# Kernel tuning notes

Measured on AMD Instinct MI355X. Metric: run time of the kernel, lower is better.

The kernel has to match this reference:

```python
import jax, jax.numpy as jnp
import numpy as np

# dims: M=512 new tokens, N=2048 model dim, D=128 head dim, H=16 heads,
# L=4096 cache length, P=2048 cache write offset

def setup_inputs() -> dict:
    key = jax.random.key(0)
    k0, k1, k2, k3 = jax.random.split(key, 4)
    M, N, D, L = 512, 2048, 128, 4096
    X = jax.random.normal(k0, (M, N), jnp.float32)
    # scale weights ~1/sqrt(N) so projections have unit-ish scale
    W_qkv = jax.random.normal(k1, (N, 3 * N), jnp.float32) * (N ** -0.5)
    H = N // D
    cache_K = jax.random.normal(k2, (H, L, D), jnp.float32)
    # realistic cache state: keys stored in cache are RMS-normalized
    cache_K = cache_K * jax.lax.rsqrt(jnp.mean(cache_K * cache_K, axis=-1, keepdims=True))
    cache_V = jax.random.normal(k3, (H, L, D), jnp.float32)
    return {"X": X, "W_qkv": W_qkv, "cache_K": cache_K, "cache_V": cache_V, "P": 2048}


def reference(X, W_qkv, cache_K, cache_V, P):
    M = X.shape[0]
    H, L, D = cache_K.shape
    qkv = X @ W_qkv                              # [M, 3N]
    q, k, v = jnp.split(qkv, 3, axis=-1)         # each [M, N]
    q = q.reshape(M, H, D).transpose(1, 0, 2)    # [H, M, D]
    k = k.reshape(M, H, D).transpose(1, 0, 2)
    v = v.reshape(M, H, D).transpose(1, 0, 2)
    # RMS-style normalization (no learned gain, no eps in original)
    q = q * jax.lax.rsqrt(jnp.mean(q * q, axis=-1, keepdims=True))
    k = k * jax.lax.rsqrt(jnp.mean(k * k, axis=-1, keepdims=True))
    # scatter-update into KV cache at position P
    Kc = jax.lax.dynamic_update_slice(cache_K, k, (0, P, 0))  # [H, L, D]
    Vc = jax.lax.dynamic_update_slice(cache_V, v, (0, P, 0))
    # unmasked, unscaled attention over the full cache (faithful to original:
    # plain exp/sum, no max-subtraction, no 1/sqrt(D))
    scores = jnp.einsum('hmd,hld->hml', q, Kc)   # [H, M, L]
    w = jnp.exp(scores)
    w = w / jnp.sum(w, axis=-1, keepdims=True)
    out = jnp.einsum('hml,hld->hmd', w, Vc)      # [H, M, D]
    return out.transpose(1, 0, 2).reshape(M, H * D)
```

## Files before the change

### kernel.cpp

```cpp
#include <hip/hip_runtime.h>
#include <math.h>

typedef _Float16 half_t;
typedef _Float16 half8 __attribute__((ext_vector_type(8)));
typedef _Float16 half4_t __attribute__((ext_vector_type(4)));
typedef _Float16 half2_t __attribute__((ext_vector_type(2)));
typedef float floatx4 __attribute__((ext_vector_type(4)));

#define M_TOK 512
#define N_DIM 2048
#define D_HEAD 128
#define H_HEADS 16
#define L_CACHE 4096
#define THREE_N 6144
#define NCHUNK 16
#define LCHUNK 256

__global__ __launch_bounds__(256) void prep_kernel(const float* __restrict__ cV,
                                                   const float* __restrict__ W,
                                                   const float* __restrict__ X,
                                                   half_t* __restrict__ V16T,
                                                   half_t* __restrict__ W16T,
                                                   half_t* __restrict__ X16) {
    __shared__ half_t tile[128 * 36];
    int b = blockIdx.x;
    int t = threadIdx.x;

    if (b < 1024) {
        size_t i = ((size_t)b * 256 + t) * 4;
        float4 v = *(const float4*)(X + i);
        half4_t h = {(half_t)v.x, (half_t)v.y, (half_t)v.z, (half_t)v.w};
        *(half4_t*)(X16 + i) = h;
        return;
    }
    b -= 1024;
    if (b < 2048) {
        int h = b >> 7;
        int rem = b & 127;
        int l0 = (rem >> 2) * 128, d0 = (rem & 3) * 32;
        {
            int row = t >> 1, q = (t & 1) * 16;
            const float* src = cV + ((size_t)h * L_CACHE + l0 + row) * D_HEAD + d0 + q;
#pragma unroll
            for (int i = 0; i < 4; ++i) {
                float4 v = *(const float4*)(src + 4 * i);
                half4_t hv = {(half_t)v.x, (half_t)v.y, (half_t)v.z, (half_t)v.w};
                *(half4_t*)&tile[row * 36 + q + 4 * i] = hv;
            }
        }
        __syncthreads();
        {
            int drow = t >> 3, seg = (t & 7) * 16;
#pragma unroll
            for (int j = 0; j < 2; ++j) {
                half8 o;
#pragma unroll
                for (int kk = 0; kk < 8; ++kk)
                    o[kk] = tile[(seg + j * 8 + kk) * 36 + drow];
                *(half8*)(V16T + ((size_t)h * D_HEAD + d0 + drow) * L_CACHE + l0 + seg + j * 8) = o;
            }
        }
        return;
    }
    b -= 2048;
    {
        int kt = b / 192, nt = b % 192;
        int k0 = kt * 128, n0 = nt * 32;
        {
            int row = t >> 1, q = (t & 1) * 16;
            const float* src = W + (size_t)(k0 + row) * THREE_N + n0 + q;
#pragma unroll
            for (int i = 0; i < 4; ++i) {
                float4 v = *(const float4*)(src + 4 * i);
                half4_t hv = {(half_t)v.x, (half_t)v.y, (half_t)v.z, (half_t)v.w};
                *(half4_t*)&tile[row * 36 + q + 4 * i] = hv;
            }
        }
        __syncthreads();
        {
            int nrow = t >> 3, seg = (t & 7) * 16;
#pragma unroll
            for (int j = 0; j < 2; ++j) {
                half8 o;
#pragma unroll
                for (int kk = 0; kk < 8; ++kk)
                    o[kk] = tile[(seg + j * 8 + kk) * 36 + nrow];
                *(half8*)(W16T + (size_t)(n0 + nrow) * N_DIM + k0 + seg + j * 8) = o;
            }
        }
    }
}

__global__ __launch_bounds__(256) void gemm_fused_kernel(const half_t* __restrict__ X16,
                                                         const half_t* __restrict__ W16T,
                                                         const int* __restrict__ Pp,
                                                         half_t* __restrict__ Q16,
                                                         float* __restrict__ cacheK,
                                                         half_t* __restrict__ V16T) {
    __shared__ half_t smem[64 * 72 + 128 * 72];
    __shared__ float ssbuf[4][32];
    half_t* As = smem;
    half_t* Bs = smem + 64 * 72;
    half_t* Vt = smem;
    const int t = threadIdx.x;
    const int wid = t >> 6, lane = t & 63;
    const int quad = lane >> 4, ln = lane & 15;
    const int bx = blockIdx.x, by = blockIdx.y;
    const int m0 = by * 64, n0 = bx * 128;
    const int wm = (wid >> 1) * 32, wn = (wid & 1) * 64;

    floatx4 acc[2][4] = {};

    const int ar = t >> 3, ag = (t & 7) * 8;
    const int br = t >> 3, bg = (t & 7) * 8;

    for (int k0 = 0; k0 < N_DIM; k0 += 64) {
        __syncthreads();
#pragma unroll
        for (int p = 0; p < 2; ++p) {
            int r = ar + p * 32;
            *(half8*)&As[r * 72 + ag] =
                *(const half8*)(X16 + (size_t)(m0 + r) * N_DIM + k0 + ag);
        }
#pragma unroll
        for (int p = 0; p < 4; ++p) {
            int r = br + p * 32;
            *(half8*)&Bs[r * 72 + bg] =
                *(const half8*)(W16T + (size_t)(n0 + r) * N_DIM + k0 + bg);
        }
        __syncthreads();
#pragma unroll
        for (int kt = 0; kt < 2; ++kt) {
            half8 a[2], b[4];
#pragma unroll
            for (int i = 0; i < 2; ++i)
                a[i] = *(half8*)&As[(wm + i * 16 + ln) * 72 + kt * 32 + quad * 8];
#pragma unroll
            for (int j = 0; j < 4; ++j)
                b[j] = *(half8*)&Bs[(wn + j * 16 + ln) * 72 + kt * 32 + quad * 8];
#pragma unroll
            for (int i = 0; i < 2; ++i)
#pragma unroll
                for (int j = 0; j < 4; ++j)
                    acc[i][j] = __builtin_amdgcn_mfma_f32_16x16x32_f16(a[i], b[j], acc[i][j], 0, 0, 0);
        }
    }

    const int seg = bx >> 4, h = bx & 15;
    const int P = *Pp;

    if (seg < 2) {
        float ss[2][4], scale[2][4];
#pragma unroll
        for (int i = 0; i < 2; ++i)
#pragma unroll
            for (int r = 0; r < 4; ++r) {
                float s = 0.f;
#pragma unroll
                for (int j = 0; j < 4; ++j) s += acc[i][j][r] * acc[i][j][r];
#pragma unroll
                for (int msk = 1; msk < 16; msk <<= 1) s += __shfl_xor(s, msk, 64);
                ss[i][r] = s;
            }
        if (ln == 0) {
#pragma unroll
            for (int i = 0; i < 2; ++i)
#pragma unroll
                for (int r = 0; r < 4; ++r)
                    ssbuf[wid][i * 16 + quad * 4 + r] = ss[i][r];
        }
        __syncthreads();
#pragma unroll
        for (int i = 0; i < 2; ++i)
#pragma unroll
            for (int r = 0; r < 4; ++r)
                scale[i][r] =
                    rsqrtf((ss[i][r] + ssbuf[wid ^ 1][i * 16 + quad * 4 + r]) * (1.0f / 128.0f));
#pragma unroll
        for (int i = 0; i < 2; ++i) {
            int mbase = m0 + wm + i * 16 + quad * 4;
#pragma unroll
            for (int j = 0; j < 4; ++j) {
                int col = wn + j * 16 + ln;
#pragma unroll
                for (int r = 0; r < 4; ++r) {
                    int m = mbase + r;
                    float v = acc[i][j][r] * scale[i][r];
                    if (seg == 0)
                        Q16[((size_t)h * M_TOK + m) * D_HEAD + col] = (half_t)v;
                    else
                        cacheK[((size_t)h * L_CACHE + P + m) * D_HEAD + col] = v;
                }
            }
        }
    } else {
        __syncthreads();
#pragma unroll
        for (int i = 0; i < 2; ++i) {
            int mbase = wm + i * 16 + quad * 4;
#pragma unroll
            for (int j = 0; j < 4; ++j) {
                int d = wn + j * 16 + ln;
#pragma unroll
                for (int r = 0; r < 4; ++r)
                    Vt[d * 72 + mbase + r] = (half_t)acc[i][j][r];
            }
        }
        __syncthreads();
#pragma unroll
        for (int p = 0; p < 4; ++p) {
            int s = p * 256 + t;
            int d = s >> 3, sg = s & 7;
            *(half8*)(V16T + ((size_t)h * D_HEAD + d) * L_CACHE + P + m0 + sg * 8) =
                *(half8*)&Vt[d * 72 + sg * 8];
        }
    }
}

__global__ __launch_bounds__(256) void attn_partial_kernel(const half_t* __restrict__ Q16,
                                                           const float* __restrict__ cacheK,
                                                           const half_t* __restrict__ V16T,
                                                           half_t* __restrict__ Opart,
                                                           float* __restrict__ mstat,
                                                           float* __restrict__ lstat) {
    __shared__ half_t Ks[64 * 136];
    __shared__ half_t Vs[128 * 72];
    __shared__ half_t Ps[4 * 16 * 72];
    const int t = threadIdx.x, w = t >> 6, lane = t & 63;
    const int quad = lane >> 4, ln = lane & 15;
    const int f = blockIdx.x;
    const int pair = (f >> 5) * 8 + (f & 7);
    const int c = pair >> 4, h = pair & 15;
    const int mb = ((f >> 3) & 3) * 128;
    const half_t* Qh = Q16 + (size_t)h * M_TOK * D_HEAD;
    const float* Kh = cacheK + (size_t)h * L_CACHE * D_HEAD;
    const half_t* Vh = V16T + (size_t)h * D_HEAD * L_CACHE;

    half8 qf[2][4];
#pragma unroll
    for (int s = 0; s < 2; ++s) {
        int m0 = mb + s * 64 + w * 16;
#pragma unroll
        for (int dt = 0; dt < 4; ++dt)
            qf[s][dt] = *(const half8*)(Qh + (size_t)(m0 + ln) * D_HEAD + dt * 32 + quad * 8);
    }

    floatx4 oacc[2][8] = {};
    float mrow[2][4], lrow[2][4];
#pragma unroll
    for (int s = 0; s < 2; ++s)
#pragma unroll
        for (int r = 0; r < 4; ++r) { mrow[s][r] = -INFINITY; lrow[s][r] = 0.f; }

    half_t* Pw = Ps + w * (16 * 72);

    for (int l0 = c * LCHUNK; l0 < (c + 1) * LCHUNK; l0 += 64) {
        __syncthreads();
        {
            int lr = t >> 4, ch = (t & 15) * 8;
#pragma unroll
            for (int p = 0; p < 4; ++p, lr += 16) {
                const float* src = Kh + (size_t)(l0 + lr) * D_HEAD + ch;
                float4 a = *(const float4*)src;
                float4 bq = *(const float4*)(src + 4);
                half8 hv = {(half_t)a.x, (half_t)a.y, (half_t)a.z, (half_t)a.w,
                            (half_t)bq.x, (half_t)bq.y, (half_t)bq.z, (half_t)bq.w};
                *(half8*)&Ks[lr * 136 + ch] = hv;
            }
        }
        {
            int dr = t >> 3, ch = t & 7;
#pragma unroll
            for (int p = 0; p < 4; ++p, dr += 32)
                *(half8*)&Vs[dr * 72 + ch * 8] =
                    *(const half8*)(Vh + (size_t)dr * L_CACHE + l0 + ch * 8);
        }
        __syncthreads();

#pragma unroll
        for (int s = 0; s < 2; ++s) {
            floatx4 sacc[4] = {};
#pragma unroll
            for (int nt = 0; nt < 4; ++nt)
#pragma unroll
                for (int dt = 0; dt < 4; ++dt) {
                    half8 b = *(half8*)&Ks[(nt * 16 + ln) * 136 + dt * 32 + quad * 8];
                    sacc[nt] = __builtin_amdgcn_mfma_f32_16x16x32_f16(qf[s][dt], b, sacc[nt], 0, 0, 0);
                }

            float alpha[4];
#pragma unroll
            for (int r = 0; r < 4; ++r) {
                float mx = fmaxf(fmaxf(sacc[0][r], sacc[1][r]), fmaxf(sacc[2][r], sacc[3][r]));
#pragma unroll
                for (int msk = 8; msk; msk >>= 1) mx = fmaxf(mx, __shfl_xor(mx, msk, 16));
                float mnew = fmaxf(mrow[s][r], mx);
                alpha[r] = __expf(mrow[s][r] - mnew);
                mrow[s][r] = mnew;
                float psum = 0.f;
#pragma unroll
                for (int nt = 0; nt < 4; ++nt) {
                    float p = __expf(sacc[nt][r] - mnew);
                    sacc[nt][r] = p;
                    psum += p;
                }
#pragma unroll
                for (int msk = 8; msk; msk >>= 1) psum += __shfl_xor(psum, msk, 16);
                lrow[s][r] = lrow[s][r] * alpha[r] + psum;
            }

#pragma unroll
            for (int nt = 0; nt < 4; ++nt)
#pragma unroll
                for (int r = 0; r < 4; ++r)
                    Pw[(quad * 4 + r) * 72 + nt * 16 + ln] = (half_t)sacc[nt][r];

#pragma unroll
            for (int nt8 = 0; nt8 < 8; ++nt8)
#pragma unroll
                for (int r = 0; r < 4; ++r)
                    oacc[s][nt8][r] *= alpha[r];

#pragma unroll
            for (int kt = 0; kt < 2; ++kt) {
                half8 a = *(half8*)&Pw[ln * 72 + kt * 32 + quad * 8];
#pragma unroll
                for (int nt8 = 0; nt8 < 8; ++nt8) {
                    half8 b = *(half8*)&Vs[(nt8 * 16 + ln) * 72 + kt * 32 + quad * 8];
                    oacc[s][nt8] = __builtin_amdgcn_mfma_f32_16x16x32_f16(a, b, oacc[s][nt8], 0, 0, 0);
                }
            }
        }
    }

    half_t* Oc = Opart + ((size_t)(c * H_HEADS + h) * M_TOK) * D_HEAD;
    float* ms = mstat + (size_t)(c * H_HEADS + h) * M_TOK;
    float* ls = lstat + (size_t)(c * H_HEADS + h) * M_TOK;
#pragma unroll
    for (int s = 0; s < 2; ++s) {
        int m0 = mb + s * 64 + w * 16;
#pragma unroll
        for (int nt8 = 0; nt8 < 8; ++nt8) {
            int col = nt8 * 16 + ln;
#pragma unroll
            for (int r = 0; r < 4; ++r)
                Oc[(size_t)(m0 + quad * 4 + r) * D_HEAD + col] = (half_t)oacc[s][nt8][r];
        }
        if (ln == 0) {
#pragma unroll
            for (int r = 0; r < 4; ++r) {
                ms[m0 + quad * 4 + r] = mrow[s][r];
                ls[m0 + quad * 4 + r] = lrow[s][r];
            }
        }
    }
}

__global__ __launch_bounds__(256) void combine_kernel(const half_t* __restrict__ Opart,
                                                      const float* __restrict__ mstat,
                                                      const float* __restrict__ lstat,
                                                      float* __restrict__ out) {
    int gw = blockIdx.x * 4 + (threadIdx.x >> 6);
    int lane = threadIdx.x & 63;
    int h = gw >> 9, m = gw & 511;
    int d = lane * 2;

    float ms[NCHUNK];
    float mg = -INFINITY;
#pragma unroll
    for (int c = 0; c < NCHUNK; ++c) {
        ms[c] = mstat[((c * H_HEADS + h) << 9) + m];
        mg = fmaxf(mg, ms[c]);
    }
    float denom = 0.f, o0 = 0.f, o1 = 0.f;
#pragma unroll
    for (int c = 0; c < NCHUNK; ++c) {
        float e = __expf(ms[c] - mg);
        denom += lstat[((c * H_HEADS + h) << 9) + m] * e;
        const half_t* Oc = Opart + (((size_t)(c * H_HEADS + h) << 9) + m) * D_HEAD + d;
        half2_t v = *(const half2_t*)Oc;
        o0 += (float)v.x * e;
        o1 += (float)v.y * e;
    }
    float inv = 1.0f / denom;
    float* op = out + (size_t)m * N_DIM + h * D_HEAD + d;
    op[0] = o0 * inv;
    op[1] = o1 * inv;
}

extern "C" void kernel_launch(void* const* d_in, const int* in_sizes, int n_in,
                              void* d_out, int out_size, void* d_ws, size_t ws_size,
                              hipStream_t stream) {
    const float* X = (const float*)d_in[0];
    const float* W = (const float*)d_in[1];
    float* cK = (float*)d_in[2];
    const float* cV = (const float*)d_in[3];
    const int* Pp = (const int*)d_in[4];
    float* out = (float*)d_out;

    char* ws = (char*)d_ws;
    half_t* Q16 = (half_t*)(ws + 0);
    half_t* V16T = (half_t*)(ws + 2097152);
    half_t* X16 = (half_t*)(ws + 18874368);
    half_t* W16T = (half_t*)(ws + 20971520);
    half_t* Opart = (half_t*)(ws + 20971520);
    float* mstat = (float*)(ws + 54525952);
    float* lstat = (float*)(ws + 55050240);

    prep_kernel<<<6144, 256, 0, stream>>>(cV, W, X, V16T, W16T, X16);
    gemm_fused_kernel<<<dim3(48, 8), 256, 0, stream>>>(X16, W16T, Pp, Q16, cK, V16T);
    attn_partial_kernel<<<1024, 256, 0, stream>>>(Q16, cK, V16T, Opart, mstat, lstat);
    combine_kernel<<<2048, 256, 0, stream>>>(Opart, mstat, lstat, out);
}
```

Measured before the change: 261.5 us.

## Convert K cache to fp16 workspace and share one LDS buffer for K and V

Adds a prep pass that converts the whole fp32 K cache to an fp16 workspace copy. The projection kernel now writes normalized K into that copy instead of the input cache, so attention reads fp16 K directly without converting in the loop. Attention also reuses one shared-memory buffer for the K and V tiles, computing both query sub-blocks' scores before loading V, which adds barriers. Total traffic likely rises: the prep pass reads 32MB and writes 16MB, while attention previously read fp32 K only once per head-chunk across four m-blocks.

```diff
diff --git a/kernel.cpp b/kernel.cpp
--- a/kernel.cpp
+++ b/kernel.cpp
@@ -16,9 +16,11 @@
 #define NCHUNK 16
 #define LCHUNK 256
 
-__global__ __launch_bounds__(256) void prep_kernel(const float* __restrict__ cV,
+__global__ __launch_bounds__(256) void prep_kernel(const float* __restrict__ cK,
+                                                   const float* __restrict__ cV,
                                                    const float* __restrict__ W,
                                                    const float* __restrict__ X,
+                                                   half_t* __restrict__ K16,
                                                    half_t* __restrict__ V16T,
                                                    half_t* __restrict__ W16T,
                                                    half_t* __restrict__ X16) {
@@ -26,6 +28,14 @@
     int b = blockIdx.x;
     int t = threadIdx.x;
 
+    if (b < 8192) {
+        size_t i = ((size_t)b * 256 + t) * 4;
+        float4 v = *(const float4*)(cK + i);
+        half4_t h = {(half_t)v.x, (half_t)v.y, (half_t)v.z, (half_t)v.w};
+        *(half4_t*)(K16 + i) = h;
+        return;
+    }
+    b -= 8192;
     if (b < 1024) {
         size_t i = ((size_t)b * 256 + t) * 4;
         float4 v = *(const float4*)(X + i);
@@ -95,7 +105,7 @@
                                                          const half_t* __restrict__ W16T,
                                                          const int* __restrict__ Pp,
                                                          half_t* __restrict__ Q16,
-                                                         float* __restrict__ cacheK,
+                                                         half_t* __restrict__ K16,
                                                          half_t* __restrict__ V16T) {
     __shared__ half_t smem[64 * 72 + 128 * 72];
     __shared__ float ssbuf[4][32];
@@ -185,11 +195,11 @@
 #pragma unroll
                 for (int r = 0; r < 4; ++r) {
                     int m = mbase + r;
-                    float v = acc[i][j][r] * scale[i][r];
+                    half_t val = (half_t)(acc[i][j][r] * scale[i][r]);
                     if (seg == 0)
-                        Q16[((size_t)h * M_TOK + m) * D_HEAD + col] = (half_t)v;
+                        Q16[((size_t)h * M_TOK + m) * D_HEAD + col] = val;
                     else
-                        cacheK[((size_t)h * L_CACHE + P + m) * D_HEAD + col] = v;
+                        K16[((size_t)h * L_CACHE + P + m) * D_HEAD + col] = val;
                 }
             }
         }
@@ -218,13 +228,12 @@
 }
 
 __global__ __launch_bounds__(256) void attn_partial_kernel(const half_t* __restrict__ Q16,
-                                                           const float* __restrict__ cacheK,
+                                                           const half_t* __restrict__ K16,
                                                            const half_t* __restrict__ V16T,
                                                            half_t* __restrict__ Opart,
                                                            float* __restrict__ mstat,
                                                            float* __restrict__ lstat) {
-    __shared__ half_t Ks[64 * 136];
-    __shared__ half_t Vs[128 * 72];
+    __shared__ half_t KV[9216];
     __shared__ half_t Ps[4 * 16 * 72];
     const int t = threadIdx.x, w = t >> 6, lane = t & 63;
     const int quad = lane >> 4, ln = lane & 15;
@@ -233,7 +242,7 @@
     const int c = pair >> 4, h = pair & 15;
     const int mb = ((f >> 3) & 3) * 128;
     const half_t* Qh = Q16 + (size_t)h * M_TOK * D_HEAD;
-    const float* Kh = cacheK + (size_t)h * L_CACHE * D_HEAD;
+    const half_t* Kh = K16 + (size_t)h * L_CACHE * D_HEAD;
     const half_t* Vh = V16T + (size_t)h * D_HEAD * L_CACHE;
 
     half8 qf[2][4];
@@ -257,76 +266,78 @@
     for (int l0 = c * LCHUNK; l0 < (c + 1) * LCHUNK; l0 += 64) {
         __syncthreads();
         {
-            int lr = t >> 4, ch = (t & 15) * 8;
-#pragma unroll
-            for (int p = 0; p < 4; ++p, lr += 16) {
-                const float* src = Kh + (size_t)(l0 + lr) * D_HEAD + ch;
-                float4 a = *(const float4*)src;
-                float4 bq = *(const float4*)(src + 4);
-                half8 hv = {(half_t)a.x, (half_t)a.y, (half_t)a.z, (half_t)a.w,
-                            (half_t)bq.x, (half_t)bq.y, (half_t)bq.z, (half_t)bq.w};
-                *(half8*)&Ks[lr * 136 + ch] = hv;
-            }
-        }
-        {
-            int dr = t >> 3, ch = t & 7;
-#pragma unroll
-            for (int p = 0; p < 4; ++p, dr += 32)
-                *(half8*)&Vs[dr * 72 + ch * 8] =
-                    *(const half8*)(Vh + (size_t)dr * L_CACHE + l0 + ch * 8);
-        }
-        __syncthreads();
-
-#pragma unroll
-        for (int s = 0; s < 2; ++s) {
-            floatx4 sacc[4] = {};
-#pragma unroll
-            for (int nt = 0; nt < 4; ++nt)
-#pragma unroll
-                for (int dt = 0; dt < 4; ++dt) {
-                    half8 b = *(half8*)&Ks[(nt * 16 + ln) * 136 + dt * 32 + quad * 8];
-                    sacc[nt] = __builtin_amdgcn_mfma_f32_16x16x32_f16(qf[s][dt], b, sacc[nt], 0, 0, 0);
-                }
-
-            float alpha[4];
+            int lr = t >> 4, ch = t & 15;
+#pragma unroll
+            for (int p = 0; p < 4; ++p, lr += 16)
+                *(half8*)&KV[lr * 136 + ch * 8] =
+                    *(const half8*)(Kh + (size_t)(l0 + lr) * D_HEAD + ch * 8);
+        }
+        __syncthreads();
+
+        floatx4 sacc[2][4] = {};
+#pragma unroll
+        for (int nt = 0; nt < 4; ++nt)
+#pragma unroll
+            for (int dt = 0; dt < 4; ++dt) {
+                half8 b = *(half8*)&KV[(nt * 16 + ln) * 136 + dt * 32 + quad * 8];
+                sacc[0][nt] = __builtin_amdgcn_mfma_f32_16x16x32_f16(qf[0][dt], b, sacc[0][nt], 0, 0, 0);
+                sacc[1][nt] = __builtin_amdgcn_mfma_f32_16x16x32_f16(qf[1][dt], b, sacc[1][nt], 0, 0, 0);
+            }
+
+        float alpha[2][4];
+#pragma unroll
+        for (int s = 0; s < 2; ++s)
 #pragma unroll
             for (int r = 0; r < 4; ++r) {
-                float mx = fmaxf(fmaxf(sacc[0][r], sacc[1][r]), fmaxf(sacc[2][r], sacc[3][r]));
+                float mx = fmaxf(fmaxf(sacc[s][0][r], sacc[s][1][r]),
+                                 fmaxf(sacc[s][2][r], sacc[s][3][r]));
 #pragma unroll
                 for (int msk = 8; msk; msk >>= 1) mx = fmaxf(mx, __shfl_xor(mx, msk, 16));
                 float mnew = fmaxf(mrow[s][r], mx);
-                alpha[r] = __expf(mrow[s][r] - mnew);
+                alpha[s][r] = __expf(mrow[s][r] - mnew);
                 mrow[s][r] = mnew;
                 float psum = 0.f;
 #pragma unroll
                 for (int nt = 0; nt < 4; ++nt) {
-                    float p = __expf(sacc[nt][r] - mnew);
-                    sacc[nt][r] = p;
+                    float p = __expf(sacc[s][nt][r] - mnew);
+                    sacc[s][nt][r] = p;
                     psum += p;
                 }
 #pragma unroll
                 for (int msk = 8; msk; msk >>= 1) psum += __shfl_xor(psum, msk, 16);
-                lrow[s][r] = lrow[s][r] * alpha[r] + psum;
-            }
-
+                lrow[s][r] = lrow[s][r] * alpha[s][r] + psum;
+            }
+
+        __syncthreads();
+        {
+            int dr = t >> 3, ch = t & 7;
+#pragma unroll
+            for (int p = 0; p < 4; ++p, dr += 32)
+                *(half8*)&KV[dr * 72 + ch * 8] =
+                    *(const half8*)(Vh + (size_t)dr * L_CACHE + l0 + ch * 8);
+        }
+        __syncthreads();
+
+#pragma unroll
+        for (int s = 0; s < 2; ++s) {
 #pragma unroll
             for (int nt = 0; nt < 4; ++nt)
 #pragma unroll
                 for (int r = 0; r < 4; ++r)
-                    Pw[(quad * 4 + r) * 72 + nt * 16 + ln] = (half_t)sacc[nt][r];
+                    Pw[(quad * 4 + r) * 72 + nt * 16 + ln] = (half_t)sacc[s][nt][r];
 
 #pragma unroll
             for (int nt8 = 0; nt8 < 8; ++nt8)
 #pragma unroll
                 for (int r = 0; r < 4; ++r)
-                    oacc[s][nt8][r] *= alpha[r];
+                    oacc[s][nt8][r] *= alpha[s][r];
 
 #pragma unroll
             for (int kt = 0; kt < 2; ++kt) {
                 half8 a = *(half8*)&Pw[ln * 72 + kt * 32 + quad * 8];
 #pragma unroll
                 for (int nt8 = 0; nt8 < 8; ++nt8) {
-                    half8 b = *(half8*)&Vs[(nt8 * 16 + ln) * 72 + kt * 32 + quad * 8];
+                    half8 b = *(half8*)&KV[(nt8 * 16 + ln) * 72 + kt * 32 + quad * 8];
                     oacc[s][nt8] = __builtin_amdgcn_mfma_f32_16x16x32_f16(a, b, oacc[s][nt8], 0, 0, 0);
                 }
             }
@@ -393,22 +404,23 @@
                               hipStream_t stream) {
     const float* X = (const float*)d_in[0];
     const float* W = (const float*)d_in[1];
-    float* cK = (float*)d_in[2];
+    const float* cK = (const float*)d_in[2];
     const float* cV = (const float*)d_in[3];
     const int* Pp = (const int*)d_in[4];
     float* out = (float*)d_out;
 
     char* ws = (char*)d_ws;
     half_t* Q16 = (half_t*)(ws + 0);
-    half_t* V16T = (half_t*)(ws + 2097152);
-    half_t* X16 = (half_t*)(ws + 18874368);
-    half_t* W16T = (half_t*)(ws + 20971520);
-    half_t* Opart = (half_t*)(ws + 20971520);
-    float* mstat = (float*)(ws + 54525952);
-    float* lstat = (float*)(ws + 55050240);
-
-    prep_kernel<<<6144, 256, 0, stream>>>(cV, W, X, V16T, W16T, X16);
-    gemm_fused_kernel<<<dim3(48, 8), 256, 0, stream>>>(X16, W16T, Pp, Q16, cK, V16T);
-    attn_partial_kernel<<<1024, 256, 0, stream>>>(Q16, cK, V16T, Opart, mstat, lstat);
+    half_t* K16 = (half_t*)(ws + 2097152);
+    half_t* V16T = (half_t*)(ws + 18874368);
+    half_t* X16 = (half_t*)(ws + 35651584);
+    half_t* W16T = (half_t*)(ws + 37748736);
+    half_t* Opart = (half_t*)(ws + 37748736);
+    float* mstat = (float*)(ws + 71303168);
+    float* lstat = (float*)(ws + 71827456);
+
+    prep_kernel<<<14336, 256, 0, stream>>>(cK, cV, W, X, K16, V16T, W16T, X16);
+    gemm_fused_kernel<<<dim3(48, 8), 256, 0, stream>>>(X16, W16T, Pp, Q16, K16, V16T);
+    attn_partial_kernel<<<1024, 256, 0, stream>>>(Q16, K16, V16T, Opart, mstat, lstat);
     combine_kernel<<<2048, 256, 0, stream>>>(Opart, mstat, lstat, out);
 }
```

Result: faster. 254.7 us (-2.6%).
